# Kernel tuning notes

Hardware: AMD Instinct MI355X
Metric: run time of the kernel (lower is better)

Reference implementation:

```python
import jax, jax.numpy as jnp
import numpy as np
import math

B, S, H, DK = 16, 4096, 16, 64
DM = H * DK          # 1024, d_model
QD = 1024            # q_d_model
KVD = 1024           # kv_d_model
MASK_P = 0.85        # randbool probability


def setup_inputs() -> dict:
    key = jax.random.key(0)
    ks = jax.random.split(key, 12)
    s = 0.02
    return {
        "q": jax.random.normal(ks[0], (B, 1, QD), jnp.float32),
        "k": jax.random.normal(ks[1], (B, S, KVD), jnp.float32),
        "v": jax.random.normal(ks[2], (B, S, KVD), jnp.float32),
        "Wq": jax.random.normal(ks[3], (QD, DM), jnp.float32) * s,
        "bq": jnp.zeros((DM,), jnp.float32),
        "Wk": jax.random.normal(ks[4], (KVD, DM), jnp.float32) * s,
        "bk": jnp.zeros((DM,), jnp.float32),
        "Wv": jax.random.normal(ks[5], (KVD, DM), jnp.float32) * s,
        "bv": jnp.zeros((DM,), jnp.float32),
        "Wo": jax.random.normal(ks[6], (DM, QD), jnp.float32) * s,
        "bo": jnp.zeros((QD,), jnp.float32),
        # randbool(shape, p=0.85): True where rand < p -> score zeroed
        "maskfill": jax.random.uniform(ks[7], (B, H, 1, S)) < MASK_P,
    }


def reference(q, k, v, Wq, bq, Wk, bk, Wv, bv, Wo, bo, maskfill):
    bs = q.shape[0]
    # projections -> [B, L, H, DK] -> [B, H, L, DK]
    qh = (q @ Wq + bq).reshape(bs, -1, H, DK).transpose(0, 2, 1, 3)  # [B,H,1,DK]
    kh = (k @ Wk + bk).reshape(bs, -1, H, DK).transpose(0, 2, 1, 3)  # [B,H,S,DK]
    vh = (v @ Wv + bv).reshape(bs, -1, H, DK).transpose(0, 2, 1, 3)  # [B,H,S,DK]

    scores1 = jnp.einsum("bhqd,bhkd->bhqk", qh, kh) / math.sqrt(DK)  # [B,H,1,S]

    # plain path (dropout = identity in eval)
    attn = jax.nn.softmax(scores1, axis=-1)
    out_h = jnp.einsum("bhqk,bhkd->bhqd", attn, vh)                  # [B,H,1,DK]

    # masked path: zero-fill (not -inf) masked raw scores, then softmax
    masked_scores = jnp.where(maskfill, 0.0, scores1)
    mattn = jax.nn.softmax(masked_scores, axis=-1)
    mout_h = jnp.einsum("bhqk,bhkd->bhqd", mattn, vh)

    concat = out_h.transpose(0, 2, 1, 3).reshape(bs, DM)
    mconcat = mout_h.transpose(0, 2, 1, 3).reshape(bs, DM)
    output = concat @ Wo + bo
    masked_output = mconcat @ Wo + bo
    return (output, masked_output)
```

## Files before the change

kernel.cpp:

```cpp
#include <hip/hip_runtime.h>
#include <stdint.h>

#define NB 16
#define NS 4096
#define NH 16
#define NC 1024

#define OFF_QHP   0u
#define OFF_QK    262144u
#define OFF_QB    524288u
#define OFF_FLAG  524544u
#define OFF_SP    524608u
#define OFF_S     557376u
#define OFF_ATT   557888u
#define OFF_CTXP  2655040u
#define OFF_CTX   11043648u
#define OFF_CON   11567936u

__global__ void k_maskprobe(const uint32_t* __restrict__ m, int* __restrict__ flag) {
    __shared__ int sf, sg;
    if (threadIdx.x == 0) { sf = 0; sg = 0; }
    __syncthreads();
    uint32_t x = m[threadIdx.x];
    if (x == 0x3F800000u) atomicOr(&sf, 1);
    else if (x > 1u) atomicOr(&sg, 1);
    __syncthreads();
    if (threadIdx.x == 0) *flag = sf ? 2 : (sg ? 1 : 0);
}

__global__ __launch_bounds__(128) void k_qh(
    const float* __restrict__ q, const float* __restrict__ Wq, float* __restrict__ qhp)
{
    __shared__ float qs[64*16];
    int dz = blockIdx.x, cs = blockIdx.y;
    int tid = threadIdx.x;
    int d = dz*128 + tid;
#pragma unroll
    for (int j = 0; j < 2; ++j) {
        int idx = j*128 + tid;
        int b = idx >> 4, c4 = (idx & 15) << 2;
        float4 t = *(const float4*)(q + (size_t)b*NC + cs*64 + c4);
        qs[(c4+0)*16 + b] = t.x; qs[(c4+1)*16 + b] = t.y;
        qs[(c4+2)*16 + b] = t.z; qs[(c4+3)*16 + b] = t.w;
    }
    __syncthreads();
    float acc[16];
#pragma unroll
    for (int b = 0; b < 16; ++b) acc[b] = 0.f;
#pragma unroll 4
    for (int c = 0; c < 64; ++c) {
        float w = Wq[(size_t)(cs*64 + c)*NC + d];
        const float4* qr = (const float4*)(qs + c*16);
        float4 q0 = qr[0], q1 = qr[1], q2 = qr[2], q3 = qr[3];
        acc[0]  = fmaf(w, q0.x, acc[0]);  acc[1]  = fmaf(w, q0.y, acc[1]);
        acc[2]  = fmaf(w, q0.z, acc[2]);  acc[3]  = fmaf(w, q0.w, acc[3]);
        acc[4]  = fmaf(w, q1.x, acc[4]);  acc[5]  = fmaf(w, q1.y, acc[5]);
        acc[6]  = fmaf(w, q1.z, acc[6]);  acc[7]  = fmaf(w, q1.w, acc[7]);
        acc[8]  = fmaf(w, q2.x, acc[8]);  acc[9]  = fmaf(w, q2.y, acc[9]);
        acc[10] = fmaf(w, q2.z, acc[10]); acc[11] = fmaf(w, q2.w, acc[11]);
        acc[12] = fmaf(w, q3.x, acc[12]); acc[13] = fmaf(w, q3.y, acc[13]);
        acc[14] = fmaf(w, q3.z, acc[14]); acc[15] = fmaf(w, q3.w, acc[15]);
    }
#pragma unroll
    for (int b = 0; b < 16; ++b) qhp[((size_t)cs*16 + b)*NC + d] = acc[b];
}

__global__ __launch_bounds__(128) void k_qk(
    const float* __restrict__ qhp, const float* __restrict__ bq,
    const float* __restrict__ Wk, const float* __restrict__ bk,
    float* __restrict__ qko, float* __restrict__ qbv)
{
    int h = blockIdx.x;
    int c = blockIdx.y*128 + threadIdx.x;
    __shared__ float qs[16*64];
    for (int j = 0; j < 8; ++j) {
        int idx = j*128 + threadIdx.x;
        int b = idx >> 6, dd = idx & 63;
        float a = bq[h*64 + dd];
#pragma unroll
        for (int cs = 0; cs < 16; ++cs) a += qhp[((size_t)cs*16 + b)*NC + h*64 + dd];
        qs[idx] = a;
    }
    __syncthreads();
    const float* wr = Wk + (size_t)c*NC + h*64;
    float acc[16];
#pragma unroll
    for (int b = 0; b < 16; ++b) acc[b] = 0.f;
#pragma unroll 4
    for (int d = 0; d < 64; ++d) {
        float w = wr[d];
#pragma unroll
        for (int b = 0; b < 16; ++b) acc[b] = fmaf(qs[b*64 + d], w, acc[b]);
    }
#pragma unroll
    for (int b = 0; b < 16; ++b) qko[((size_t)b*NH + h)*NC + c] = acc[b];
    if (blockIdx.y == 0 && threadIdx.x < 16) {
        int b = threadIdx.x; float a = 0.f;
        for (int d = 0; d < 64; ++d) a = fmaf(qs[b*64 + d], bk[h*64 + d], a);
        qbv[b*NH + h] = a;
    }
}

#define QTS 20
__global__ __launch_bounds__(256) void k_scoresI(
    const float* __restrict__ kk, const float* __restrict__ qkm,
    const float* __restrict__ qbv, const void* __restrict__ mask,
    const int* __restrict__ flagp, float* __restrict__ att, float* __restrict__ Sp)
{
    __shared__ float qt[512*QTS];
    __shared__ float red[4][2][16];
    int sb = blockIdx.x, b = blockIdx.y;
    int tid = threadIdx.x;
    int ph = tid & 3, hg = (tid >> 2) & 3, rg = tid >> 4;
    int srow = sb*128 + rg*8;
    const float* kr = kk + ((size_t)b*NS + srow)*NC + ph*4;
    float acc[8][4];
#pragma unroll
    for (int i = 0; i < 8; ++i)
#pragma unroll
        for (int j = 0; j < 4; ++j) acc[i][j] = 0.f;

    for (int cz = 0; cz < 2; ++cz) {
        __syncthreads();
#pragma unroll
        for (int j = 0; j < 32; ++j) {
            int idx = j*256 + tid;
            int h = idx >> 9, c = idx & 511;
            qt[c*QTS + h] = qkm[((size_t)b*NH + h)*NC + cz*512 + c];
        }
        __syncthreads();
        const float* kc0 = kr + cz*512;
        float4 kv[8], kn[8];
#pragma unroll
        for (int i = 0; i < 8; ++i) kv[i] = *(const float4*)(kc0 + i*NC);
        for (int w = 0; w < 32; ++w) {
            if (w < 31) {
#pragma unroll
                for (int i = 0; i < 8; ++i)
                    kn[i] = *(const float4*)(kc0 + i*NC + (w+1)*16);
            }
#pragma unroll
            for (int j = 0; j < 4; ++j) {
                const float* qp = qt + (w*16 + ph*4 + j)*QTS + hg*4;
                float4 qv = *(const float4*)qp;
#pragma unroll
                for (int i = 0; i < 8; ++i) {
                    float kc = (j == 0) ? kv[i].x : (j == 1) ? kv[i].y
                             : (j == 2) ? kv[i].z : kv[i].w;
                    acc[i][0] = fmaf(kc, qv.x, acc[i][0]);
                    acc[i][1] = fmaf(kc, qv.y, acc[i][1]);
                    acc[i][2] = fmaf(kc, qv.z, acc[i][2]);
                    acc[i][3] = fmaf(kc, qv.w, acc[i][3]);
                }
            }
#pragma unroll
            for (int i = 0; i < 8; ++i) kv[i] = kn[i];
        }
    }
#pragma unroll
    for (int i = 0; i < 8; ++i)
#pragma unroll
        for (int j = 0; j < 4; ++j) {
            acc[i][j] += __shfl_xor(acc[i][j], 1, 64);
            acc[i][j] += __shfl_xor(acc[i][j], 2, 64);
        }
    float d0[4], d1[4];
    if (ph == 0) {
#pragma unroll
        for (int j = 0; j < 4; ++j) { d0[j] = acc[0][j]; d1[j] = acc[1][j]; }
    } else if (ph == 1) {
#pragma unroll
        for (int j = 0; j < 4; ++j) { d0[j] = acc[2][j]; d1[j] = acc[3][j]; }
    } else if (ph == 2) {
#pragma unroll
        for (int j = 0; j < 4; ++j) { d0[j] = acc[4][j]; d1[j] = acc[5][j]; }
    } else {
#pragma unroll
        for (int j = 0; j < 4; ++j) { d0[j] = acc[6][j]; d1[j] = acc[7][j]; }
    }
    int sA = srow + 2*ph, sB = sA + 1;
    int fl = *flagp;
    unsigned mA = 0, mB = 0;
    if (fl == 1) {
        const uint8_t* mp = (const uint8_t*)mask + (size_t)(b*NH + hg*4)*NS;
#pragma unroll
        for (int j = 0; j < 4; ++j) {
            if (mp[(size_t)j*NS + sA]) mA |= (1u << j);
            if (mp[(size_t)j*NS + sB]) mB |= (1u << j);
        }
    } else if (fl == 2) {
        const float* mp = (const float*)mask + (size_t)(b*NH + hg*4)*NS;
#pragma unroll
        for (int j = 0; j < 4; ++j) {
            if (mp[(size_t)j*NS + sA] != 0.f) mA |= (1u << j);
            if (mp[(size_t)j*NS + sB] != 0.f) mB |= (1u << j);
        }
    } else {
        const int* mp = (const int*)mask + (size_t)(b*NH + hg*4)*NS;
#pragma unroll
        for (int j = 0; j < 4; ++j) {
            if (mp[(size_t)j*NS + sA]) mA |= (1u << j);
            if (mp[(size_t)j*NS + sB]) mB |= (1u << j);
        }
    }
    float p0a[4], p1a[4], p0b[4], p1b[4], r0[4], r1[4];
#pragma unroll
    for (int j = 0; j < 4; ++j) {
        float qb = qbv[b*NH + hg*4 + j];
        float va = (d0[j] + qb) * 0.125f;
        float vb = (d1[j] + qb) * 0.125f;
        p0a[j] = __expf(va);  p1a[j] = (mA >> j & 1u) ? 1.0f : p0a[j];
        p0b[j] = __expf(vb);  p1b[j] = (mB >> j & 1u) ? 1.0f : p0b[j];
        r0[j] = p0a[j] + p0b[j];
        r1[j] = p1a[j] + p1b[j];
    }
    float* aA = att + ((size_t)b*NS + sA)*32 + hg*4;
    float* aB = att + ((size_t)b*NS + sB)*32 + hg*4;
    *(float4*)(aA)      = make_float4(p0a[0], p0a[1], p0a[2], p0a[3]);
    *(float4*)(aA + 16) = make_float4(p1a[0], p1a[1], p1a[2], p1a[3]);
    *(float4*)(aB)      = make_float4(p0b[0], p0b[1], p0b[2], p0b[3]);
    *(float4*)(aB + 16) = make_float4(p1b[0], p1b[1], p1b[2], p1b[3]);

#pragma unroll
    for (int j = 0; j < 4; ++j) {
        r0[j] += __shfl_xor(r0[j], 1, 64);  r1[j] += __shfl_xor(r1[j], 1, 64);
        r0[j] += __shfl_xor(r0[j], 2, 64);  r1[j] += __shfl_xor(r1[j], 2, 64);
        r0[j] += __shfl_xor(r0[j], 16, 64); r1[j] += __shfl_xor(r1[j], 16, 64);
        r0[j] += __shfl_xor(r0[j], 32, 64); r1[j] += __shfl_xor(r1[j], 32, 64);
    }
    int wv = tid >> 6;
    if ((tid & 51) == 0) {
#pragma unroll
        for (int j = 0; j < 4; ++j) {
            red[wv][0][hg*4 + j] = r0[j];
            red[wv][1][hg*4 + j] = r1[j];
        }
    }
    __syncthreads();
    if (tid < 32) {
        int pa = tid >> 4, h = tid & 15;
        Sp[((size_t)b*32 + sb)*32 + tid] =
            red[0][pa][h] + red[1][pa][h] + red[2][pa][h] + red[3][pa][h];
    }
}

__global__ void k_sred(const float* __restrict__ Sp, float* __restrict__ S) {
    int t = blockIdx.x*256 + threadIdx.x;
    int p = t >> 8, b = (t >> 4) & 15, h = t & 15;
    float a = 0.f;
#pragma unroll
    for (int sb = 0; sb < 32; ++sb) a += Sp[((size_t)b*32 + sb)*32 + p*16 + h];
    S[t] = a;
}

__global__ __launch_bounds__(256,2) void k_ctx(
    const float* __restrict__ v, const float* __restrict__ att, float* __restrict__ ctxp)
{
    __shared__ float al[64*32];
    __shared__ float buf[8192];
    int b = blockIdx.x & 15, ss = blockIdx.x >> 4;
    int cz = blockIdx.y;
    int tid = threadIdx.x, ct = tid & 63, rg = tid >> 6;
    int s1 = ss * 256;
    float acc[32][4];
#pragma unroll
    for (int i = 0; i < 32; ++i)
#pragma unroll
        for (int j = 0; j < 4; ++j) acc[i][j] = 0.f;

    for (int c0 = 0; c0 < 256; c0 += 64) {
        __syncthreads();
#pragma unroll
        for (int jj = 0; jj < 2; ++jj) {
            int idx = jj*256 + tid;
            ((float4*)al)[idx] = ((const float4*)(att + ((size_t)b*NS + s1 + c0)*32))[idx];
        }
        __syncthreads();
        for (int it = 0; it < 16; ++it) {
            int rl = c0 + it*4 + rg;
            float4 vv = *(const float4*)(v + ((size_t)b*NS + s1 + rl)*NC + cz*256 + ct*4);
            const float4* ar = (const float4*)(al + (it*4 + rg)*32);
#pragma unroll
            for (int u = 0; u < 8; ++u) {
                float4 aw = ar[u];
                acc[u*4+0][0] = fmaf(aw.x, vv.x, acc[u*4+0][0]);
                acc[u*4+0][1] = fmaf(aw.x, vv.y, acc[u*4+0][1]);
                acc[u*4+0][2] = fmaf(aw.x, vv.z, acc[u*4+0][2]);
                acc[u*4+0][3] = fmaf(aw.x, vv.w, acc[u*4+0][3]);
                acc[u*4+1][0] = fmaf(aw.y, vv.x, acc[u*4+1][0]);
                acc[u*4+1][1] = fmaf(aw.y, vv.y, acc[u*4+1][1]);
                acc[u*4+1][2] = fmaf(aw.y, vv.z, acc[u*4+1][2]);
                acc[u*4+1][3] = fmaf(aw.y, vv.w, acc[u*4+1][3]);
                acc[u*4+2][0] = fmaf(aw.z, vv.x, acc[u*4+2][0]);
                acc[u*4+2][1] = fmaf(aw.z, vv.y, acc[u*4+2][1]);
                acc[u*4+2][2] = fmaf(aw.z, vv.z, acc[u*4+2][2]);
                acc[u*4+2][3] = fmaf(aw.z, vv.w, acc[u*4+2][3]);
                acc[u*4+3][0] = fmaf(aw.w, vv.x, acc[u*4+3][0]);
                acc[u*4+3][1] = fmaf(aw.w, vv.y, acc[u*4+3][1]);
                acc[u*4+3][2] = fmaf(aw.w, vv.z, acc[u*4+3][2]);
                acc[u*4+3][3] = fmaf(aw.w, vv.w, acc[u*4+3][3]);
            }
        }
    }
    for (int pr = 0; pr < 4; ++pr) {
        __syncthreads();
#pragma unroll
        for (int u = 0; u < 8; ++u) {
            int ph = pr*8 + u;
            float4 t; t.x = acc[ph][0]; t.y = acc[ph][1]; t.z = acc[ph][2]; t.w = acc[ph][3];
            ((float4*)buf)[(rg*8 + u)*64 + ct] = t;
        }
        __syncthreads();
#pragma unroll
        for (int kx = 0; kx < 2; ++kx) {
            int i = kx*256 + tid;
            int u2 = i >> 6, c2 = i & 63;
            float4 s = ((float4*)buf)[(size_t)(0*8 + u2)*64 + c2];
#pragma unroll
            for (int r2 = 1; r2 < 4; ++r2) {
                float4 t = ((float4*)buf)[(size_t)(r2*8 + u2)*64 + c2];
                s.x += t.x; s.y += t.y; s.z += t.z; s.w += t.w;
            }
            int ph = pr*8 + u2, p = ph >> 4, h = ph & 15;
            *(float4*)(ctxp + ((((size_t)ss*2 + p)*NB + b)*NH + h)*NC + cz*256 + c2*4) = s;
        }
    }
}

__global__ void k_ctxred(const float* __restrict__ ctxp, const float* __restrict__ S,
                         float* __restrict__ ctx) {
    size_t i = (size_t)blockIdx.x * 256 + threadIdx.x;
    float a = 0.f;
#pragma unroll
    for (int ss = 0; ss < 16; ++ss) a += ctxp[(size_t)ss*524288 + i];
    ctx[i] = a / S[i >> 10];
}

__global__ __launch_bounds__(256) void k_outh(
    const float* __restrict__ ctx, const float* __restrict__ Wv,
    const float* __restrict__ bv, float* __restrict__ con)
{
    int b = blockIdx.y, p = blockIdx.z;
    int d = blockIdx.x*256 + threadIdx.x;
    int h0 = blockIdx.x*4;
    __shared__ float cl[4*NC];
    for (int i = threadIdx.x; i < 4*NC; i += 256)
        cl[i] = ctx[(((size_t)p*NB + b)*NH + h0 + (i >> 10))*NC + (i & 1023)];
    __syncthreads();
    const float* c2 = cl + ((threadIdx.x >> 6) << 10);
    float a0=0.f,a1=0.f,a2=0.f,a3=0.f;
    for (int c = 0; c < NC; c += 4) {
        a0 = fmaf(c2[c+0], Wv[(size_t)(c+0)*NC + d], a0);
        a1 = fmaf(c2[c+1], Wv[(size_t)(c+1)*NC + d], a1);
        a2 = fmaf(c2[c+2], Wv[(size_t)(c+2)*NC + d], a2);
        a3 = fmaf(c2[c+3], Wv[(size_t)(c+3)*NC + d], a3);
    }
    con[((size_t)p*NB + b)*NC + d] = (a0+a1)+(a2+a3) + bv[d];
}

__global__ __launch_bounds__(256) void k_out(
    const float* __restrict__ con, const float* __restrict__ Wo,
    const float* __restrict__ bo, float* __restrict__ out)
{
    int b = blockIdx.y, p = blockIdx.z;
    int o = blockIdx.x*256 + threadIdx.x;
    __shared__ float cl[NC];
    for (int i = threadIdx.x; i < NC; i += 256)
        cl[i] = con[((size_t)p*NB + b)*NC + i];
    __syncthreads();
    float a0=0.f,a1=0.f,a2=0.f,a3=0.f;
    for (int m = 0; m < NC; m += 4) {
        a0 = fmaf(cl[m+0], Wo[(size_t)(m+0)*NC + o], a0);
        a1 = fmaf(cl[m+1], Wo[(size_t)(m+1)*NC + o], a1);
        a2 = fmaf(cl[m+2], Wo[(size_t)(m+2)*NC + o], a2);
        a3 = fmaf(cl[m+3], Wo[(size_t)(m+3)*NC + o], a3);
    }
    out[(size_t)p*NB*NC + (size_t)b*NC + o] = (a0+a1)+(a2+a3) + bo[o];
}

extern "C" void kernel_launch(void* const* d_in, const int* in_sizes, int n_in,
                              void* d_out, int out_size, void* d_ws, size_t ws_size,
                              hipStream_t stream)
{
    (void)in_sizes; (void)n_in; (void)out_size; (void)ws_size;
    const float* q  = (const float*)d_in[0];
    const float* k  = (const float*)d_in[1];
    const float* v  = (const float*)d_in[2];
    const float* Wq = (const float*)d_in[3];
    const float* bq = (const float*)d_in[4];
    const float* Wk = (const float*)d_in[5];
    const float* bk = (const float*)d_in[6];
    const float* Wv = (const float*)d_in[7];
    const float* bv = (const float*)d_in[8];
    const float* Wo = (const float*)d_in[9];
    const float* bo = (const float*)d_in[10];
    const void*  mk = d_in[11];

    float* ws   = (float*)d_ws;
    float* qhp  = ws + OFF_QHP;
    float* qkv  = ws + OFF_QK;
    float* qbv  = ws + OFF_QB;
    int*   flg  = (int*)(ws + OFF_FLAG);
    float* Sp   = ws + OFF_SP;
    float* S    = ws + OFF_S;
    float* att  = ws + OFF_ATT;
    float* ctxp = ws + OFF_CTXP;
    float* ctx  = ws + OFF_CTX;
    float* con  = ws + OFF_CON;
    float* out  = (float*)d_out;

    k_maskprobe<<<1, 1024, 0, stream>>>((const uint32_t*)mk, flg);
    k_qh<<<dim3(8, 16), 128, 0, stream>>>(q, Wq, qhp);
    k_qk<<<dim3(16, 8), 128, 0, stream>>>(qhp, bq, Wk, bk, qkv, qbv);
    k_scoresI<<<dim3(32, 16), 256, 0, stream>>>(k, qkv, qbv, mk, flg, att, Sp);
    k_sred<<<2, 256, 0, stream>>>(Sp, S);
    k_ctx<<<dim3(256, 4), 256, 0, stream>>>(v, att, ctxp);
    k_ctxred<<<2048, 256, 0, stream>>>(ctxp, S, ctx);
    k_outh<<<dim3(4, NB, 2), 256, 0, stream>>>(ctx, Wv, bv, con);
    k_out<<<dim3(4, NB, 2), 256, 0, stream>>>(con, Wo, bo, out);
}
```

Before: 311.3 us.

## Fuse mask probe, score sum and ctx reduction into neighbouring kernels; deepen K prefetch

The mask-type probe is moved into every scores block, which reads the first 128 bytes itself. The separate softmax-denominator reduction and ctx partial-reduction kernels are folded into the output-projection kernel, so three launches go away along with the intermediate ctx/S buffers. The K-tile loop in the scores kernel now prefetches two steps ahead using a triple-buffered register rotation. In exchange, the reductions in k_outhN run on only 128 blocks and re-read partial sums redundantly, and the deeper prefetch raises register pressure.

Measured after the change: 309.8 us. Within noise of the previous version (-0.5%).

```diff
diff --git a/kernel.cpp b/kernel.cpp
--- a/kernel.cpp
+++ b/kernel.cpp
@@ -9,24 +9,10 @@
 #define OFF_QHP   0u
 #define OFF_QK    262144u
 #define OFF_QB    524288u
-#define OFF_FLAG  524544u
 #define OFF_SP    524608u
-#define OFF_S     557376u
-#define OFF_ATT   557888u
-#define OFF_CTXP  2655040u
-#define OFF_CTX   11043648u
-#define OFF_CON   11567936u
-
-__global__ void k_maskprobe(const uint32_t* __restrict__ m, int* __restrict__ flag) {
-    __shared__ int sf, sg;
-    if (threadIdx.x == 0) { sf = 0; sg = 0; }
-    __syncthreads();
-    uint32_t x = m[threadIdx.x];
-    if (x == 0x3F800000u) atomicOr(&sf, 1);
-    else if (x > 1u) atomicOr(&sg, 1);
-    __syncthreads();
-    if (threadIdx.x == 0) *flag = sf ? 2 : (sg ? 1 : 0);
-}
+#define OFF_ATT   540992u
+#define OFF_CTXP  2638144u
+#define OFF_CON   11026752u
 
 __global__ __launch_bounds__(128) void k_qh(
     const float* __restrict__ q, const float* __restrict__ Wq, float* __restrict__ qhp)
@@ -102,10 +88,25 @@
 }
 
 #define QTS 20
-__global__ __launch_bounds__(256) void k_scoresI(
+#define SCOMP(BUF, W)                                                          \
+    _Pragma("unroll")                                                          \
+    for (int j = 0; j < 4; ++j) {                                              \
+        const float* qp = qt + ((W)*16 + ph*4 + j)*QTS + hg*4;                 \
+        float4 qv = *(const float4*)qp;                                        \
+        _Pragma("unroll")                                                      \
+        for (int i = 0; i < 8; ++i) {                                          \
+            float kc = (j == 0) ? BUF[i].x : (j == 1) ? BUF[i].y               \
+                     : (j == 2) ? BUF[i].z : BUF[i].w;                         \
+            acc[i][0] = fmaf(kc, qv.x, acc[i][0]);                             \
+            acc[i][1] = fmaf(kc, qv.y, acc[i][1]);                             \
+            acc[i][2] = fmaf(kc, qv.z, acc[i][2]);                             \
+            acc[i][3] = fmaf(kc, qv.w, acc[i][3]);                             \
+        }                                                                      \
+    }
+__global__ __launch_bounds__(256) void k_scoresI2(
     const float* __restrict__ kk, const float* __restrict__ qkm,
     const float* __restrict__ qbv, const void* __restrict__ mask,
-    const int* __restrict__ flagp, float* __restrict__ att, float* __restrict__ Sp)
+    float* __restrict__ att, float* __restrict__ Sp)
 {
     __shared__ float qt[512*QTS];
     __shared__ float red[4][2][16];
@@ -113,6 +114,24 @@
     int tid = threadIdx.x;
     int ph = tid & 3, hg = (tid >> 2) & 3, rg = tid >> 4;
     int srow = sb*128 + rg*8;
+
+    int fl;
+    {
+        const uint4* mw = (const uint4*)mask;
+        unsigned f = 0u, g = 0u;
+#pragma unroll
+        for (int j = 0; j < 8; ++j) {
+            uint4 m4 = mw[j];
+            f |= (m4.x == 0x3F800000u) | (m4.y == 0x3F800000u)
+               | (m4.z == 0x3F800000u) | (m4.w == 0x3F800000u);
+            g |= ((m4.x > 1u) & (m4.x != 0x3F800000u))
+               | ((m4.y > 1u) & (m4.y != 0x3F800000u))
+               | ((m4.z > 1u) & (m4.z != 0x3F800000u))
+               | ((m4.w > 1u) & (m4.w != 0x3F800000u));
+        }
+        fl = f ? 2 : (g ? 1 : 0);
+    }
+
     const float* kr = kk + ((size_t)b*NS + srow)*NC + ph*4;
     float acc[8][4];
 #pragma unroll
@@ -130,31 +149,26 @@
         }
         __syncthreads();
         const float* kc0 = kr + cz*512;
-        float4 kv[8], kn[8];
-#pragma unroll
-        for (int i = 0; i < 8; ++i) kv[i] = *(const float4*)(kc0 + i*NC);
-        for (int w = 0; w < 32; ++w) {
-            if (w < 31) {
+        float4 A[8], B[8], T[8];
+#pragma unroll
+        for (int i = 0; i < 8; ++i) A[i] = *(const float4*)(kc0 + i*NC);
+#pragma unroll
+        for (int i = 0; i < 8; ++i) B[i] = *(const float4*)(kc0 + i*NC + 16);
+        for (int w = 0; w < 32; w += 2) {
+            if (w + 2 < 32) {
 #pragma unroll
                 for (int i = 0; i < 8; ++i)
-                    kn[i] = *(const float4*)(kc0 + i*NC + (w+1)*16);
+                    T[i] = *(const float4*)(kc0 + i*NC + (w+2)*16);
             }
-#pragma unroll
-            for (int j = 0; j < 4; ++j) {
-                const float* qp = qt + (w*16 + ph*4 + j)*QTS + hg*4;
-                float4 qv = *(const float4*)qp;
-#pragma unroll
-                for (int i = 0; i < 8; ++i) {
-                    float kc = (j == 0) ? kv[i].x : (j == 1) ? kv[i].y
-                             : (j == 2) ? kv[i].z : kv[i].w;
-                    acc[i][0] = fmaf(kc, qv.x, acc[i][0]);
-                    acc[i][1] = fmaf(kc, qv.y, acc[i][1]);
-                    acc[i][2] = fmaf(kc, qv.z, acc[i][2]);
-                    acc[i][3] = fmaf(kc, qv.w, acc[i][3]);
-                }
+            SCOMP(A, w);
+            if (w + 3 < 32) {
+#pragma unroll
+                for (int i = 0; i < 8; ++i)
+                    A[i] = *(const float4*)(kc0 + i*NC + (w+3)*16);
             }
-#pragma unroll
-            for (int i = 0; i < 8; ++i) kv[i] = kn[i];
+            SCOMP(B, (w+1));
+#pragma unroll
+            for (int i = 0; i < 8; ++i) { B[i] = A[i]; A[i] = T[i]; }
         }
     }
 #pragma unroll
@@ -179,7 +193,6 @@
         for (int j = 0; j < 4; ++j) { d0[j] = acc[6][j]; d1[j] = acc[7][j]; }
     }
     int sA = srow + 2*ph, sB = sA + 1;
-    int fl = *flagp;
     unsigned mA = 0, mB = 0;
     if (fl == 1) {
         const uint8_t* mp = (const uint8_t*)mask + (size_t)(b*NH + hg*4)*NS;
@@ -242,15 +255,6 @@
         Sp[((size_t)b*32 + sb)*32 + tid] =
             red[0][pa][h] + red[1][pa][h] + red[2][pa][h] + red[3][pa][h];
     }
-}
-
-__global__ void k_sred(const float* __restrict__ Sp, float* __restrict__ S) {
-    int t = blockIdx.x*256 + threadIdx.x;
-    int p = t >> 8, b = (t >> 4) & 15, h = t & 15;
-    float a = 0.f;
-#pragma unroll
-    for (int sb = 0; sb < 32; ++sb) a += Sp[((size_t)b*32 + sb)*32 + p*16 + h];
-    S[t] = a;
 }
 
 __global__ __launch_bounds__(256,2) void k_ctx(
@@ -327,25 +331,34 @@
     }
 }
 
-__global__ void k_ctxred(const float* __restrict__ ctxp, const float* __restrict__ S,
-                         float* __restrict__ ctx) {
-    size_t i = (size_t)blockIdx.x * 256 + threadIdx.x;
-    float a = 0.f;
-#pragma unroll
-    for (int ss = 0; ss < 16; ++ss) a += ctxp[(size_t)ss*524288 + i];
-    ctx[i] = a / S[i >> 10];
-}
-
-__global__ __launch_bounds__(256) void k_outh(
-    const float* __restrict__ ctx, const float* __restrict__ Wv,
-    const float* __restrict__ bv, float* __restrict__ con)
+__global__ __launch_bounds__(256) void k_outhN(
+    const float* __restrict__ ctxp, const float* __restrict__ Sp,
+    const float* __restrict__ Wv, const float* __restrict__ bv,
+    float* __restrict__ con)
 {
     int b = blockIdx.y, p = blockIdx.z;
-    int d = blockIdx.x*256 + threadIdx.x;
-    int h0 = blockIdx.x*4;
+    int dx = blockIdx.x;
+    int d = dx*256 + threadIdx.x;
+    int h0 = dx*4;
     __shared__ float cl[4*NC];
-    for (int i = threadIdx.x; i < 4*NC; i += 256)
-        cl[i] = ctx[(((size_t)p*NB + b)*NH + h0 + (i >> 10))*NC + (i & 1023)];
+    float Sinv[4];
+#pragma unroll
+    for (int j = 0; j < 4; ++j) {
+        float a = 0.f;
+        for (int sb = 0; sb < 32; ++sb)
+            a += Sp[((size_t)b*32 + sb)*32 + p*16 + h0 + j];
+        Sinv[j] = 1.f / a;
+    }
+#pragma unroll
+    for (int hh = 0; hh < 4; ++hh) {
+        for (int cc = threadIdx.x; cc < NC; cc += 256) {
+            float a = 0.f;
+#pragma unroll
+            for (int ss = 0; ss < 16; ++ss)
+                a += ctxp[((((size_t)ss*2 + p)*NB + b)*NH + h0 + hh)*NC + cc];
+            cl[hh*NC + cc] = a * Sinv[hh];
+        }
+    }
     __syncthreads();
     const float* c2 = cl + ((threadIdx.x >> 6) << 10);
     float a0=0.f,a1=0.f,a2=0.f,a3=0.f;
@@ -400,22 +413,16 @@
     float* qhp  = ws + OFF_QHP;
     float* qkv  = ws + OFF_QK;
     float* qbv  = ws + OFF_QB;
-    int*   flg  = (int*)(ws + OFF_FLAG);
     float* Sp   = ws + OFF_SP;
-    float* S    = ws + OFF_S;
     float* att  = ws + OFF_ATT;
     float* ctxp = ws + OFF_CTXP;
-    float* ctx  = ws + OFF_CTX;
     float* con  = ws + OFF_CON;
     float* out  = (float*)d_out;
 
-    k_maskprobe<<<1, 1024, 0, stream>>>((const uint32_t*)mk, flg);
     k_qh<<<dim3(8, 16), 128, 0, stream>>>(q, Wq, qhp);
     k_qk<<<dim3(16, 8), 128, 0, stream>>>(qhp, bq, Wk, bk, qkv, qbv);
-    k_scoresI<<<dim3(32, 16), 256, 0, stream>>>(k, qkv, qbv, mk, flg, att, Sp);
-    k_sred<<<2, 256, 0, stream>>>(Sp, S);
+    k_scoresI2<<<dim3(32, 16), 256, 0, stream>>>(k, qkv, qbv, mk, att, Sp);
     k_ctx<<<dim3(256, 4), 256, 0, stream>>>(v, att, ctxp);
-    k_ctxred<<<2048, 256, 0, stream>>>(ctxp, S, ctx);
-    k_outh<<<dim3(4, NB, 2), 256, 0, stream>>>(ctx, Wv, bv, con);
+    k_outhN<<<dim3(4, NB, 2), 256, 0, stream>>>(ctxp, Sp, Wv, bv, con);
     k_out<<<dim3(4, NB, 2), 256, 0, stream>>>(con, Wo, bo, out);
 }
```
